# Kernel optimization log

Measured on AMD Instinct MI355X. Metric: run time of the kernel, lower is better.

The kernel has to match this reference:

```python
import jax, jax.numpy as jnp
import numpy as np

B = 1024       # batch of graphs
NUM = 512      # predicates / nodes per graph
D = 64         # embedding_dim
H = 64         # hidden_dim
E = 4096       # edges per graph (shared structure across batch)
MAIN_NUM = 10  # softmax segment [0, MAIN_NUM); sigmoid on the rest


def setup_inputs() -> dict:
    key = jax.random.key(0)
    ks = jax.random.split(key, 8)
    x = jax.random.uniform(ks[0], (B, NUM), dtype=jnp.float32)
    embedding = jax.random.normal(ks[1], (NUM, D), dtype=jnp.float32) * 0.1
    W1 = jax.random.normal(ks[2], (D, H), dtype=jnp.float32) * (1.0 / np.sqrt(D))
    b1 = jnp.zeros((H,), jnp.float32)
    W2 = jax.random.normal(ks[3], (H, H), dtype=jnp.float32) * (1.0 / np.sqrt(H))
    b2 = jnp.zeros((H,), jnp.float32)
    W3 = jax.random.normal(ks[4], (H, 1), dtype=jnp.float32) * (1.0 / np.sqrt(H))
    b3 = jnp.zeros((1,), jnp.float32)
    edge_row = jax.random.randint(ks[5], (E,), 0, NUM, dtype=jnp.int32)
    edge_col = jax.random.randint(ks[6], (E,), 0, NUM, dtype=jnp.int32)
    return {"x": x, "embedding": embedding, "W1": W1, "b1": b1,
            "W2": W2, "b2": b2, "W3": W3, "b3": b3,
            "edge_row": edge_row, "edge_col": edge_col}


def _gcn_layer(h, W, b, row, col, norm):
    # h: [B, NUM, in]; GCNConv = linear -> D^{-1/2} A D^{-1/2} aggregate -> +bias
    hW = jnp.einsum('bni,io->bno', h, W)                 # [B, NUM, out]
    msg = hW[:, row, :] * norm[None, :, None]            # [B, E, out]
    agg = jnp.zeros_like(hW).at[:, col, :].add(msg)      # scatter to targets
    return agg + b


def reference(x, embedding, W1, b1, W2, b2, W3, b3, edge_row, edge_col):
    num = x.shape[1]
    # symmetric GCN normalization (add_self_loops=False, unit edge weights)
    deg = jnp.zeros((num,), x.dtype).at[edge_col].add(1.0)
    dinv = jnp.where(deg > 0, jax.lax.rsqrt(jnp.maximum(deg, 1.0)), 0.0)
    norm = dinv[edge_row] * dinv[edge_col]               # [E]

    h = x[..., None] * embedding                         # [B, NUM, D]
    h = jax.nn.relu(_gcn_layer(h, W1, b1, edge_row, edge_col, norm))
    h = jax.nn.relu(_gcn_layer(h, W2, b2, edge_row, edge_col, norm))
    logits = _gcn_layer(h, W3, b3, edge_row, edge_col, norm)[..., 0]  # [B, NUM]

    # convert_to_confidence: softmax over multiclass segment, sigmoid elsewhere
    phi_sm = jax.nn.softmax(logits[:, :MAIN_NUM], axis=1)
    phi_sg = jax.nn.sigmoid(logits[:, MAIN_NUM:])
    return jnp.concatenate([phi_sm, phi_sg], axis=1)
```

## Files before the change

### kernel.cpp

```cpp
#include <hip/hip_runtime.h>
#include <stdint.h>

#define NB    1024
#define NUM   512
#define HD    64
#define NE    4096
#define MAIN  10
#define HBS   72

typedef __attribute__((ext_vector_type(8))) short short8;
typedef __attribute__((ext_vector_type(4))) float f32x4;

__device__ __forceinline__ short f2bf(float f) {
    uint32_t u = __float_as_uint(f);
    u += 0x7fffu + ((u >> 16) & 1u);
    return (short)(u >> 16);
}
__device__ __forceinline__ float bf2f(short s) {
    return __uint_as_float(((uint32_t)(uint16_t)s) << 16);
}

__global__ __launch_bounds__(512) void prep_all(
    const int* __restrict__ erow, const int* __restrict__ ecol,
    const float* __restrict__ emb, const float* __restrict__ W1,
    const float* __restrict__ W2,
    int* __restrict__ rsptr, int* __restrict__ colmap, int* __restrict__ epk,
    short* __restrict__ E1, short* __restrict__ W2T)
{
    const int t = threadIdx.x;
    if (blockIdx.x != 0) {
        int g = (blockIdx.x - 1) * 512 + t;
        if (g < NUM * HD) {
            int node = g >> 6, dim = g & 63;
            float acc = 0.0f;
            #pragma unroll
            for (int k = 0; k < HD; ++k) acc += emb[node * HD + k] * W1[k * HD + dim];
            E1[g] = f2bf(acc);
        } else if (g < NUM * HD + HD * HD) {
            int j = g - NUM * HD;
            int dout = j >> 6, din = j & 63;
            W2T[j] = f2bf(W2[din * HD + dout]);
        }
        return;
    }

    __shared__ int   sdeg[NUM];
    __shared__ int   aux[NUM];
    __shared__ float sdinv[NUM];
    __shared__ int   rankof[NUM];
    __shared__ int   curs[NUM];
    __shared__ int   rdeg[NUM];

    sdeg[t] = 0;
    __syncthreads();
    for (int e = t; e < NE; e += 512) atomicAdd(&sdeg[ecol[e]], 1);
    __syncthreads();
    const int deg = sdeg[t];
    const int dbin = deg < NUM ? deg : NUM - 1;
    sdinv[t] = deg > 0 ? rsqrtf((float)deg) : 0.0f;
    aux[t] = 0;
    __syncthreads();
    atomicAdd(&aux[dbin], 1);
    __syncthreads();
    for (int ofs = 1; ofs < NUM; ofs <<= 1) {
        int v = (t >= ofs) ? aux[t - ofs] : 0;
        __syncthreads();
        aux[t] += v;
        __syncthreads();
    }
    curs[t] = (t == 0) ? 0 : aux[t - 1];
    __syncthreads();
    const int r = atomicAdd(&curs[dbin], 1);
    rankof[t] = r;
    rdeg[r]   = deg;
    colmap[r] = t;
    __syncthreads();
    for (int ofs = 1; ofs < NUM; ofs <<= 1) {
        int v = (t >= ofs) ? rdeg[t - ofs] : 0;
        __syncthreads();
        rdeg[t] += v;
        __syncthreads();
    }
    rsptr[t] = (t == 0) ? 0 : rdeg[t - 1];
    if (t == NUM - 1) rsptr[NUM] = rdeg[NUM - 1];
    __syncthreads();
    const int myrank = rankof[t];
    curs[t] = (myrank == 0) ? 0 : rdeg[myrank - 1];
    __syncthreads();
    for (int e = t; e < NE; e += 512) {
        int c = ecol[e], rr = erow[e];
        int p = atomicAdd(&curs[c], 1);
        unsigned nb = (unsigned short)f2bf(sdinv[rr] * sdinv[c]);
        epk[p] = (rr << 16) | (int)nb;
    }
}

__global__ __launch_bounds__(1024, 4) void gcn_all(
    const float* __restrict__ x, const short* __restrict__ E1,
    const short* __restrict__ W2T,
    const float* __restrict__ b1, const float* __restrict__ b2,
    const float* __restrict__ W3, const float* __restrict__ b3,
    const int* __restrict__ rsptrg, const int* __restrict__ colmapg,
    const int* __restrict__ epkg,
    float* __restrict__ out)
{
    __shared__ short HA[NUM * HD];
    __shared__ short HB[NUM * HBS];
    __shared__ int   eps[NE];
    __shared__ int   sptr[513];
    __shared__ int   scm[NUM];
    __shared__ float sred[2];

    float* tv   = (float*)HB;
    float* slog = ((float*)HB) + NUM;

    const int t    = threadIdx.x;
    const int b    = blockIdx.x;
    const int lane = t & 63;
    const int wave = t >> 6;
    const int q    = lane >> 4;
    const int l15  = lane & 15;
    const int grp  = lane >> 3;
    const int dbase = (lane & 7) * 8;

    *(int4*)&eps[t * 4] = *(const int4*)&epkg[t * 4];
    if (t < 513) sptr[t] = rsptrg[t];
    if (t < NUM) scm[t] = colmapg[t];

    #pragma unroll
    for (int p = 0; p < 4; ++p) {
        int i = t + p * 1024;
        int r = i >> 3, d8 = (i & 7) * 8;
        float xr = x[b * NUM + r];
        short8 e = *(const short8*)&E1[r * HD + d8];
        short8 o;
        #pragma unroll
        for (int j = 0; j < 8; ++j) o[j] = f2bf(xr * bf2f(e[j]));
        *(short8*)&HA[r * HD + d8] = o;
    }

    float b1v[8], b2v[8], w3v[8];
    {
        f32x4 u0 = *(const f32x4*)&b1[dbase], u1 = *(const f32x4*)&b1[dbase + 4];
        f32x4 v0 = *(const f32x4*)&b2[dbase], v1 = *(const f32x4*)&b2[dbase + 4];
        f32x4 w0 = *(const f32x4*)&W3[dbase], w1 = *(const f32x4*)&W3[dbase + 4];
        #pragma unroll
        for (int j = 0; j < 4; ++j) {
            b1v[j] = u0[j]; b1v[j + 4] = u1[j];
            b2v[j] = v0[j]; b2v[j + 4] = v1[j];
            w3v[j] = w0[j]; w3v[j + 4] = w1[j];
        }
    }
    __syncthreads();

#define EDGE_MAC(pe)                                                          \
    {                                                                         \
        float n = __uint_as_float((unsigned)(pe) << 16);                      \
        uint4 hv = *(const uint4*)&HA[((unsigned)(pe) >> 16) * HD + dbase];   \
        a[0] = fmaf(n, __uint_as_float(hv.x << 16), a[0]);                    \
        a[1] = fmaf(n, __uint_as_float(hv.x & 0xffff0000u), a[1]);            \
        a[2] = fmaf(n, __uint_as_float(hv.y << 16), a[2]);                    \
        a[3] = fmaf(n, __uint_as_float(hv.y & 0xffff0000u), a[3]);            \
        a[4] = fmaf(n, __uint_as_float(hv.z << 16), a[4]);                    \
        a[5] = fmaf(n, __uint_as_float(hv.z & 0xffff0000u), a[5]);            \
        a[6] = fmaf(n, __uint_as_float(hv.w << 16), a[6]);                    \
        a[7] = fmaf(n, __uint_as_float(hv.w & 0xffff0000u), a[7]);            \
    }

    #pragma unroll 1
    for (int set = 0; set < 4; ++set) {
        int r  = set * 128 + wave * 8 + grp;
        int e0 = sptr[r], e1 = sptr[r + 1];
        int c  = scm[r];
        float a[8];
        #pragma unroll
        for (int j = 0; j < 8; ++j) a[j] = 0.0f;
        int e = e0;
        for (; e + 2 <= e1; e += 2) {
            int pe0 = eps[e], pe1 = eps[e + 1];
            EDGE_MAC(pe0);
            EDGE_MAC(pe1);
        }
        if (e < e1) { int pe0 = eps[e]; EDGE_MAC(pe0); }
        short8 o;
        #pragma unroll
        for (int j = 0; j < 8; ++j) o[j] = f2bf(fmaxf(a[j] + b1v[j], 0.0f));
        *(short8*)&HB[c * HBS + dbase] = o;
    }
    __syncthreads();

    {
        short8 bfr[2][4];
        #pragma unroll
        for (int ks = 0; ks < 2; ++ks)
            #pragma unroll
            for (int nt = 0; nt < 4; ++nt)
                bfr[ks][nt] = *(const short8*)&W2T[(nt * 16 + l15) * HD + ks * 32 + q * 8];
        f32x4 acc[2][4];
        #pragma unroll
        for (int mt = 0; mt < 2; ++mt)
            #pragma unroll
            for (int nt = 0; nt < 4; ++nt) acc[mt][nt] = (f32x4){0.f, 0.f, 0.f, 0.f};
        const int mbase = wave * 32;
        #pragma unroll
        for (int mt = 0; mt < 2; ++mt)
            #pragma unroll
            for (int ks = 0; ks < 2; ++ks) {
                short8 af = *(const short8*)&HB[(mbase + mt * 16 + l15) * HBS
                                                + ks * 32 + q * 8];
                #pragma unroll
                for (int nt = 0; nt < 4; ++nt)
                    acc[mt][nt] = __builtin_amdgcn_mfma_f32_16x16x32_bf16(
                        af, bfr[ks][nt], acc[mt][nt], 0, 0, 0);
            }
        #pragma unroll
        for (int mt = 0; mt < 2; ++mt)
            #pragma unroll
            for (int nt = 0; nt < 4; ++nt)
                #pragma unroll
                for (int i = 0; i < 4; ++i)
                    HA[(mbase + mt * 16 + q * 4 + i) * HD + nt * 16 + l15] =
                        f2bf(acc[mt][nt][i]);
    }
    __syncthreads();

    #pragma unroll 1
    for (int set = 0; set < 4; ++set) {
        int r  = set * 128 + wave * 8 + grp;
        int e0 = sptr[r], e1 = sptr[r + 1];
        int c  = scm[r];
        float a[8];
        #pragma unroll
        for (int j = 0; j < 8; ++j) a[j] = 0.0f;
        int e = e0;
        for (; e + 2 <= e1; e += 2) {
            int pe0 = eps[e], pe1 = eps[e + 1];
            EDGE_MAC(pe0);
            EDGE_MAC(pe1);
        }
        if (e < e1) { int pe0 = eps[e]; EDGE_MAC(pe0); }
        float v = 0.0f;
        #pragma unroll
        for (int j = 0; j < 8; ++j)
            v += fmaxf(a[j] + b2v[j], 0.0f) * w3v[j];
        v += __shfl_xor(v, 1, 64);
        v += __shfl_xor(v, 2, 64);
        v += __shfl_xor(v, 4, 64);
        if ((lane & 7) == 0) tv[c] = v;
    }
    __syncthreads();

    if (t < NUM) {
        int e0 = sptr[t], e1 = sptr[t + 1];
        float a = 0.0f;
        for (int e = e0; e < e1; ++e) {
            unsigned pe = (unsigned)eps[e];
            a = fmaf(__uint_as_float(pe << 16), tv[pe >> 16], a);
        }
        slog[scm[t]] = a + b3[0];
    }
    __syncthreads();

    if (t < 64) {
        float v = (t < MAIN) ? slog[t] : -1e30f;
        float m = v;
        m = fmaxf(m, __shfl_xor(m, 1, 64));
        m = fmaxf(m, __shfl_xor(m, 2, 64));
        m = fmaxf(m, __shfl_xor(m, 4, 64));
        m = fmaxf(m, __shfl_xor(m, 8, 64));
        float ev = (t < MAIN) ? __expf(v - m) : 0.0f;
        ev += __shfl_xor(ev, 1, 64);
        ev += __shfl_xor(ev, 2, 64);
        ev += __shfl_xor(ev, 4, 64);
        ev += __shfl_xor(ev, 8, 64);
        if (t == 0) { sred[0] = m; sred[1] = ev; }
    }
    __syncthreads();

    if (t < NUM) {
        float l = slog[t];
        float o = (t < MAIN) ? __expf(l - sred[0]) / sred[1]
                             : 1.0f / (1.0f + __expf(-l));
        out[b * NUM + t] = o;
    }
#undef EDGE_MAC
}

extern "C" void kernel_launch(void* const* d_in, const int* in_sizes, int n_in,
                              void* d_out, int out_size, void* d_ws, size_t ws_size,
                              hipStream_t stream) {
    const float* x    = (const float*)d_in[0];
    const float* emb  = (const float*)d_in[1];
    const float* W1   = (const float*)d_in[2];
    const float* b1   = (const float*)d_in[3];
    const float* W2   = (const float*)d_in[4];
    const float* b2   = (const float*)d_in[5];
    const float* W3   = (const float*)d_in[6];
    const float* b3   = (const float*)d_in[7];
    const int*   erow = (const int*)d_in[8];
    const int*   ecol = (const int*)d_in[9];

    char* ws = (char*)d_ws;
    int*   rsptr  = (int*)ws;
    int*   colmap = (int*)(ws + 2176);
    int*   epk    = (int*)(ws + 4224);
    short* E1     = (short*)(ws + 20608);
    short* W2T    = (short*)(ws + 86144);

    prep_all<<<73, 512, 0, stream>>>(erow, ecol, emb, W1, W2,
                                     rsptr, colmap, epk, E1, W2T);
    gcn_all<<<NB, 1024, 0, stream>>>(x, E1, W2T, b1, b2, W3, b3,
                                     rsptr, colmap, epk, (float*)d_out);
}
```

Baseline: 161.5 us.

## Fuse graph preprocessing and first-layer linear into single per-batch kernel

Removes the separate prep kernel and its workspace. Each block now builds the degree-sorted CSR edge list in shared memory, using wave-shuffle scans. It also computes the first linear layer (x*emb)@W1 per graph with MFMA, where before it scaled a precomputed emb@W1 table. W1 and W2 are read and converted to bf16 directly from global memory. This drops a kernel launch and the serialization between the two kernels, but every one of the 1024 blocks now repeats the graph preprocessing plus an extra MFMA GEMM, and it does strided uncoalesced weight loads.

```diff
diff --git a/kernel.cpp b/kernel.cpp
--- a/kernel.cpp
+++ b/kernel.cpp
@@ -20,88 +20,12 @@
     return __uint_as_float(((uint32_t)(uint16_t)s) << 16);
 }
 
-__global__ __launch_bounds__(512) void prep_all(
-    const int* __restrict__ erow, const int* __restrict__ ecol,
-    const float* __restrict__ emb, const float* __restrict__ W1,
-    const float* __restrict__ W2,
-    int* __restrict__ rsptr, int* __restrict__ colmap, int* __restrict__ epk,
-    short* __restrict__ E1, short* __restrict__ W2T)
-{
-    const int t = threadIdx.x;
-    if (blockIdx.x != 0) {
-        int g = (blockIdx.x - 1) * 512 + t;
-        if (g < NUM * HD) {
-            int node = g >> 6, dim = g & 63;
-            float acc = 0.0f;
-            #pragma unroll
-            for (int k = 0; k < HD; ++k) acc += emb[node * HD + k] * W1[k * HD + dim];
-            E1[g] = f2bf(acc);
-        } else if (g < NUM * HD + HD * HD) {
-            int j = g - NUM * HD;
-            int dout = j >> 6, din = j & 63;
-            W2T[j] = f2bf(W2[din * HD + dout]);
-        }
-        return;
-    }
-
-    __shared__ int   sdeg[NUM];
-    __shared__ int   aux[NUM];
-    __shared__ float sdinv[NUM];
-    __shared__ int   rankof[NUM];
-    __shared__ int   curs[NUM];
-    __shared__ int   rdeg[NUM];
-
-    sdeg[t] = 0;
-    __syncthreads();
-    for (int e = t; e < NE; e += 512) atomicAdd(&sdeg[ecol[e]], 1);
-    __syncthreads();
-    const int deg = sdeg[t];
-    const int dbin = deg < NUM ? deg : NUM - 1;
-    sdinv[t] = deg > 0 ? rsqrtf((float)deg) : 0.0f;
-    aux[t] = 0;
-    __syncthreads();
-    atomicAdd(&aux[dbin], 1);
-    __syncthreads();
-    for (int ofs = 1; ofs < NUM; ofs <<= 1) {
-        int v = (t >= ofs) ? aux[t - ofs] : 0;
-        __syncthreads();
-        aux[t] += v;
-        __syncthreads();
-    }
-    curs[t] = (t == 0) ? 0 : aux[t - 1];
-    __syncthreads();
-    const int r = atomicAdd(&curs[dbin], 1);
-    rankof[t] = r;
-    rdeg[r]   = deg;
-    colmap[r] = t;
-    __syncthreads();
-    for (int ofs = 1; ofs < NUM; ofs <<= 1) {
-        int v = (t >= ofs) ? rdeg[t - ofs] : 0;
-        __syncthreads();
-        rdeg[t] += v;
-        __syncthreads();
-    }
-    rsptr[t] = (t == 0) ? 0 : rdeg[t - 1];
-    if (t == NUM - 1) rsptr[NUM] = rdeg[NUM - 1];
-    __syncthreads();
-    const int myrank = rankof[t];
-    curs[t] = (myrank == 0) ? 0 : rdeg[myrank - 1];
-    __syncthreads();
-    for (int e = t; e < NE; e += 512) {
-        int c = ecol[e], rr = erow[e];
-        int p = atomicAdd(&curs[c], 1);
-        unsigned nb = (unsigned short)f2bf(sdinv[rr] * sdinv[c]);
-        epk[p] = (rr << 16) | (int)nb;
-    }
-}
-
-__global__ __launch_bounds__(1024, 4) void gcn_all(
-    const float* __restrict__ x, const short* __restrict__ E1,
-    const short* __restrict__ W2T,
+__global__ __launch_bounds__(1024, 4) void gcn_one(
+    const float* __restrict__ x, const float* __restrict__ emb,
+    const float* __restrict__ W1, const float* __restrict__ W2,
     const float* __restrict__ b1, const float* __restrict__ b2,
     const float* __restrict__ W3, const float* __restrict__ b3,
-    const int* __restrict__ rsptrg, const int* __restrict__ colmapg,
-    const int* __restrict__ epkg,
+    const int* __restrict__ erow, const int* __restrict__ ecol,
     float* __restrict__ out)
 {
     __shared__ short HA[NUM * HD];
@@ -109,34 +33,148 @@
     __shared__ int   eps[NE];
     __shared__ int   sptr[513];
     __shared__ int   scm[NUM];
+    __shared__ int   wsum[16];
     __shared__ float sred[2];
 
+    int*   sdeg = (int*)HB;
+    int*   aux  = sdeg + NUM;
+    float* sdv  = (float*)(aux + NUM);
+    int*   rnk  = (int*)(sdv + NUM);
+    int*   rdg  = rnk + NUM;
     float* tv   = (float*)HB;
     float* slog = ((float*)HB) + NUM;
 
-    const int t    = threadIdx.x;
-    const int b    = blockIdx.x;
-    const int lane = t & 63;
-    const int wave = t >> 6;
-    const int q    = lane >> 4;
-    const int l15  = lane & 15;
-    const int grp  = lane >> 3;
+    const int t     = threadIdx.x;
+    const int b     = blockIdx.x;
+    const int lane  = t & 63;
+    const int wave  = t >> 6;
+    const int q     = lane >> 4;
+    const int l15   = lane & 15;
+    const int grp   = lane >> 3;
     const int dbase = (lane & 7) * 8;
 
-    *(int4*)&eps[t * 4] = *(const int4*)&epkg[t * 4];
-    if (t < 513) sptr[t] = rsptrg[t];
-    if (t < NUM) scm[t] = colmapg[t];
-
-    #pragma unroll
-    for (int p = 0; p < 4; ++p) {
-        int i = t + p * 1024;
-        int r = i >> 3, d8 = (i & 7) * 8;
-        float xr = x[b * NUM + r];
-        short8 e = *(const short8*)&E1[r * HD + d8];
-        short8 o;
-        #pragma unroll
-        for (int j = 0; j < 8; ++j) o[j] = f2bf(xr * bf2f(e[j]));
-        *(short8*)&HA[r * HD + d8] = o;
+    if (t < NUM) { sdeg[t] = 0; aux[t] = 0; }
+    __syncthreads();
+    for (int e = t; e < NE; e += 1024) atomicAdd(&sdeg[ecol[e]], 1);
+    __syncthreads();
+    int deg = 0, dbin = 0;
+    if (t < NUM) {
+        deg  = sdeg[t];
+        dbin = deg < NUM ? deg : NUM - 1;
+        sdv[t] = deg > 0 ? rsqrtf((float)deg) : 0.0f;
+        atomicAdd(&aux[dbin], 1);
+    }
+    __syncthreads();
+    {
+        int v = (t < NUM) ? aux[t] : 0;
+        if (t < NUM) {
+            #pragma unroll
+            for (int ofs = 1; ofs < 64; ofs <<= 1) {
+                int sh = __shfl_up(v, ofs, 64);
+                if (lane >= ofs) v += sh;
+            }
+            if (lane == 63) wsum[wave] = v;
+        }
+        __syncthreads();
+        if (t == 0) {
+            int s = 0;
+            #pragma unroll
+            for (int w = 0; w < 8; ++w) { int tmp = wsum[w]; wsum[w] = s; s += tmp; }
+        }
+        __syncthreads();
+        if (t < NUM) aux[t] = v + wsum[wave];
+        __syncthreads();
+    }
+    if (t < NUM) sdeg[t] = (t == 0) ? 0 : aux[t - 1];
+    __syncthreads();
+    if (t < NUM) {
+        int r = atomicAdd(&sdeg[dbin], 1);
+        rnk[t] = r;
+        rdg[r] = deg;
+        scm[r] = t;
+    }
+    __syncthreads();
+    {
+        int dv = (t < NUM) ? rdg[t] : 0;
+        int v  = dv;
+        if (t < NUM) {
+            #pragma unroll
+            for (int ofs = 1; ofs < 64; ofs <<= 1) {
+                int sh = __shfl_up(v, ofs, 64);
+                if (lane >= ofs) v += sh;
+            }
+            if (lane == 63) wsum[wave] = v;
+        }
+        __syncthreads();
+        if (t == 0) {
+            int s = 0;
+            #pragma unroll
+            for (int w = 0; w < 8; ++w) { int tmp = wsum[w]; wsum[w] = s; s += tmp; }
+        }
+        __syncthreads();
+        if (t < NUM) {
+            int inc = v + wsum[wave];
+            sptr[t] = inc - dv;
+            if (t == NUM - 1) sptr[NUM] = inc;
+        }
+        __syncthreads();
+    }
+    if (t < NUM) aux[t] = sptr[rnk[t]];
+    __syncthreads();
+    for (int e = t; e < NE; e += 1024) {
+        int c = ecol[e], rr = erow[e];
+        int p = atomicAdd(&aux[c], 1);
+        unsigned nb = (unsigned short)f2bf(sdv[rr] * sdv[c]);
+        eps[p] = (rr << 16) | (int)nb;
+    }
+    __syncthreads();
+
+    {
+        short8 bfr[2][4];
+        #pragma unroll
+        for (int ks = 0; ks < 2; ++ks)
+            #pragma unroll
+            for (int nt = 0; nt < 4; ++nt) {
+                short8 v;
+                #pragma unroll
+                for (int j = 0; j < 8; ++j)
+                    v[j] = f2bf(W1[(ks * 32 + q * 8 + j) * HD + nt * 16 + l15]);
+                bfr[ks][nt] = v;
+            }
+        f32x4 acc[2][4];
+        #pragma unroll
+        for (int mt = 0; mt < 2; ++mt)
+            #pragma unroll
+            for (int nt = 0; nt < 4; ++nt) acc[mt][nt] = (f32x4){0.f, 0.f, 0.f, 0.f};
+        const int mbase = wave * 32;
+        #pragma unroll
+        for (int mt = 0; mt < 2; ++mt) {
+            int r = mbase + mt * 16 + l15;
+            float xr = x[b * NUM + r];
+            #pragma unroll
+            for (int ks = 0; ks < 2; ++ks) {
+                const float* ep = &emb[r * HD + ks * 32 + q * 8];
+                f32x4 e0 = *(const f32x4*)ep;
+                f32x4 e1 = *(const f32x4*)(ep + 4);
+                short8 af;
+                af[0] = f2bf(xr * e0[0]); af[1] = f2bf(xr * e0[1]);
+                af[2] = f2bf(xr * e0[2]); af[3] = f2bf(xr * e0[3]);
+                af[4] = f2bf(xr * e1[0]); af[5] = f2bf(xr * e1[1]);
+                af[6] = f2bf(xr * e1[2]); af[7] = f2bf(xr * e1[3]);
+                #pragma unroll
+                for (int nt = 0; nt < 4; ++nt)
+                    acc[mt][nt] = __builtin_amdgcn_mfma_f32_16x16x32_bf16(
+                        af, bfr[ks][nt], acc[mt][nt], 0, 0, 0);
+            }
+        }
+        #pragma unroll
+        for (int mt = 0; mt < 2; ++mt)
+            #pragma unroll
+            for (int nt = 0; nt < 4; ++nt)
+                #pragma unroll
+                for (int i = 0; i < 4; ++i)
+                    HA[(mbase + mt * 16 + q * 4 + i) * HD + nt * 16 + l15] =
+                        f2bf(acc[mt][nt][i]);
     }
 
     float b1v[8], b2v[8], w3v[8];
@@ -194,8 +232,13 @@
         #pragma unroll
         for (int ks = 0; ks < 2; ++ks)
             #pragma unroll
-            for (int nt = 0; nt < 4; ++nt)
-                bfr[ks][nt] = *(const short8*)&W2T[(nt * 16 + l15) * HD + ks * 32 + q * 8];
+            for (int nt = 0; nt < 4; ++nt) {
+                short8 v;
+                #pragma unroll
+                for (int j = 0; j < 8; ++j)
+                    v[j] = f2bf(W2[(ks * 32 + q * 8 + j) * HD + nt * 16 + l15]);
+                bfr[ks][nt] = v;
+            }
         f32x4 acc[2][4];
         #pragma unroll
         for (int mt = 0; mt < 2; ++mt)
@@ -300,15 +343,6 @@
     const int*   erow = (const int*)d_in[8];
     const int*   ecol = (const int*)d_in[9];
 
-    char* ws = (char*)d_ws;
-    int*   rsptr  = (int*)ws;
-    int*   colmap = (int*)(ws + 2176);
-    int*   epk    = (int*)(ws + 4224);
-    short* E1     = (short*)(ws + 20608);
-    short* W2T    = (short*)(ws + 86144);
-
-    prep_all<<<73, 512, 0, stream>>>(erow, ecol, emb, W1, W2,
-                                     rsptr, colmap, epk, E1, W2T);
-    gcn_all<<<NB, 1024, 0, stream>>>(x, E1, W2T, b1, b2, W3, b3,
-                                     rsptr, colmap, epk, (float*)d_out);
+    gcn_one<<<NB, 1024, 0, stream>>>(x, emb, W1, W2, b1, b2, W3, b3,
+                                     erow, ecol, (float*)d_out);
 }
```

Result: slower. 192.1 us (+19.0%).

## Pad CSR edge segments to even length and vectorize edge gathers

Applied to the files above, without the earlier changes.

Each row's edge segment is padded to an even count, with zero-filled entries that have a zero norm, so the aggregation loops can load edge words as int2 and run four edges per iteration with no odd tail. The prep kernel's scans now use wave shuffles instead of barrier-heavy shared-memory loops. The bf16 high-half unpack drops its mask, leaving the low bits as small noise. The gcn kernel reads colmap from global memory instead of staging it in LDS. The gcn kernel also loads a larger padded edge array into LDS, and the third-layer scalar loop now walks the zero padding entries too.

```diff
diff --git a/kernel.cpp b/kernel.cpp
--- a/kernel.cpp
+++ b/kernel.cpp
@@ -5,6 +5,7 @@
 #define NUM   512
 #define HD    64
 #define NE    4096
+#define NEP   4608
 #define MAIN  10
 #define HBS   72
 
@@ -46,86 +47,119 @@
 
     __shared__ int   sdeg[NUM];
     __shared__ int   aux[NUM];
-    __shared__ float sdinv[NUM];
-    __shared__ int   rankof[NUM];
-    __shared__ int   curs[NUM];
-    __shared__ int   rdeg[NUM];
-
-    sdeg[t] = 0;
+    __shared__ float sdv[NUM];
+    __shared__ int   rnk[NUM];
+    __shared__ int   rdg[NUM];
+    __shared__ int   wsum[8];
+
+    const int lane = t & 63, wv = t >> 6;
+
+    sdeg[t] = 0; aux[t] = 0;
     __syncthreads();
     for (int e = t; e < NE; e += 512) atomicAdd(&sdeg[ecol[e]], 1);
     __syncthreads();
-    const int deg = sdeg[t];
+    const int deg  = sdeg[t];
+    const int pdeg = (deg + 1) & ~1;
     const int dbin = deg < NUM ? deg : NUM - 1;
-    sdinv[t] = deg > 0 ? rsqrtf((float)deg) : 0.0f;
-    aux[t] = 0;
-    __syncthreads();
+    sdv[t] = deg > 0 ? rsqrtf((float)deg) : 0.0f;
     atomicAdd(&aux[dbin], 1);
     __syncthreads();
-    for (int ofs = 1; ofs < NUM; ofs <<= 1) {
-        int v = (t >= ofs) ? aux[t - ofs] : 0;
-        __syncthreads();
-        aux[t] += v;
-        __syncthreads();
-    }
-    curs[t] = (t == 0) ? 0 : aux[t - 1];
-    __syncthreads();
-    const int r = atomicAdd(&curs[dbin], 1);
-    rankof[t] = r;
-    rdeg[r]   = deg;
-    colmap[r] = t;
-    __syncthreads();
-    for (int ofs = 1; ofs < NUM; ofs <<= 1) {
-        int v = (t >= ofs) ? rdeg[t - ofs] : 0;
-        __syncthreads();
-        rdeg[t] += v;
-        __syncthreads();
-    }
-    rsptr[t] = (t == 0) ? 0 : rdeg[t - 1];
-    if (t == NUM - 1) rsptr[NUM] = rdeg[NUM - 1];
-    __syncthreads();
-    const int myrank = rankof[t];
-    curs[t] = (myrank == 0) ? 0 : rdeg[myrank - 1];
+    {
+        int v = aux[t];
+        #pragma unroll
+        for (int ofs = 1; ofs < 64; ofs <<= 1) {
+            int sh = __shfl_up(v, ofs, 64);
+            if (lane >= ofs) v += sh;
+        }
+        if (lane == 63) wsum[wv] = v;
+        __syncthreads();
+        if (t == 0) {
+            int s = 0;
+            #pragma unroll
+            for (int w = 0; w < 8; ++w) { int tmp = wsum[w]; wsum[w] = s; s += tmp; }
+        }
+        __syncthreads();
+        int inc = v + wsum[wv];
+        sdeg[t] = inc - ((dbin == t) ? 0 : 0);
+        aux[t]  = inc;
+        __syncthreads();
+        sdeg[t] = (t == 0) ? 0 : aux[t - 1];
+        __syncthreads();
+    }
+    {
+        int r = atomicAdd(&sdeg[dbin], 1);
+        rnk[t] = r;
+        rdg[r] = pdeg;
+        colmap[r] = t;
+    }
+    __syncthreads();
+    {
+        int dv = rdg[t], v = dv;
+        #pragma unroll
+        for (int ofs = 1; ofs < 64; ofs <<= 1) {
+            int sh = __shfl_up(v, ofs, 64);
+            if (lane >= ofs) v += sh;
+        }
+        if (lane == 63) wsum[wv] = v;
+        __syncthreads();
+        if (t == 0) {
+            int s = 0;
+            #pragma unroll
+            for (int w = 0; w < 8; ++w) { int tmp = wsum[w]; wsum[w] = s; s += tmp; }
+        }
+        __syncthreads();
+        int inc  = v + wsum[wv];
+        int excl = inc - dv;
+        rsptr[t] = excl;
+        if (t == NUM - 1) rsptr[NUM] = inc;
+        aux[t] = excl;
+        __syncthreads();
+    }
+    sdeg[t] = aux[rnk[t]];
+    __syncthreads();
+    for (int i = t; i < NEP; i += 512) epk[i] = 0;
     __syncthreads();
     for (int e = t; e < NE; e += 512) {
         int c = ecol[e], rr = erow[e];
-        int p = atomicAdd(&curs[c], 1);
-        unsigned nb = (unsigned short)f2bf(sdinv[rr] * sdinv[c]);
+        int p = atomicAdd(&sdeg[c], 1);
+        unsigned nb = (unsigned short)f2bf(sdv[rr] * sdv[c]);
         epk[p] = (rr << 16) | (int)nb;
     }
 }
 
-__global__ __launch_bounds__(1024, 4) void gcn_all(
+__global__ __launch_bounds__(1024, 4) void gcn_body(
     const float* __restrict__ x, const short* __restrict__ E1,
     const short* __restrict__ W2T,
     const float* __restrict__ b1, const float* __restrict__ b2,
     const float* __restrict__ W3, const float* __restrict__ b3,
-    const int* __restrict__ rsptrg, const int* __restrict__ colmapg,
+    const int* __restrict__ rsptrg, const int* __restrict__ colmap,
     const int* __restrict__ epkg,
     float* __restrict__ out)
 {
     __shared__ short HA[NUM * HD];
     __shared__ short HB[NUM * HBS];
-    __shared__ int   eps[NE];
+    __shared__ int   eps[NEP];
     __shared__ int   sptr[513];
-    __shared__ int   scm[NUM];
     __shared__ float sred[2];
 
     float* tv   = (float*)HB;
     float* slog = ((float*)HB) + NUM;
 
-    const int t    = threadIdx.x;
-    const int b    = blockIdx.x;
-    const int lane = t & 63;
-    const int wave = t >> 6;
-    const int q    = lane >> 4;
-    const int l15  = lane & 15;
-    const int grp  = lane >> 3;
+    const int t     = threadIdx.x;
+    const int b     = blockIdx.x;
+    const int lane  = t & 63;
+    const int wave  = t >> 6;
+    const int q     = lane >> 4;
+    const int l15   = lane & 15;
+    const int grp   = lane >> 3;
     const int dbase = (lane & 7) * 8;
 
-    *(int4*)&eps[t * 4] = *(const int4*)&epkg[t * 4];
+    {
+        const int4* g4 = (const int4*)epkg;
+        *(int4*)&eps[t * 4] = g4[t];
+        if (t < 128) *(int4*)&eps[4096 + t * 4] = g4[1024 + t];
+    }
     if (t < 513) sptr[t] = rsptrg[t];
-    if (t < NUM) scm[t] = colmapg[t];
 
     #pragma unroll
     for (int p = 0; p < 4; ++p) {
@@ -158,30 +192,33 @@
         float n = __uint_as_float((unsigned)(pe) << 16);                      \
         uint4 hv = *(const uint4*)&HA[((unsigned)(pe) >> 16) * HD + dbase];   \
         a[0] = fmaf(n, __uint_as_float(hv.x << 16), a[0]);                    \
-        a[1] = fmaf(n, __uint_as_float(hv.x & 0xffff0000u), a[1]);            \
+        a[1] = fmaf(n, __uint_as_float(hv.x), a[1]);                          \
         a[2] = fmaf(n, __uint_as_float(hv.y << 16), a[2]);                    \
-        a[3] = fmaf(n, __uint_as_float(hv.y & 0xffff0000u), a[3]);            \
+        a[3] = fmaf(n, __uint_as_float(hv.y), a[3]);                          \
         a[4] = fmaf(n, __uint_as_float(hv.z << 16), a[4]);                    \
-        a[5] = fmaf(n, __uint_as_float(hv.z & 0xffff0000u), a[5]);            \
+        a[5] = fmaf(n, __uint_as_float(hv.z), a[5]);                          \
         a[6] = fmaf(n, __uint_as_float(hv.w << 16), a[6]);                    \
-        a[7] = fmaf(n, __uint_as_float(hv.w & 0xffff0000u), a[7]);            \
+        a[7] = fmaf(n, __uint_as_float(hv.w), a[7]);                          \
     }
 
     #pragma unroll 1
     for (int set = 0; set < 4; ++set) {
         int r  = set * 128 + wave * 8 + grp;
         int e0 = sptr[r], e1 = sptr[r + 1];
-        int c  = scm[r];
+        int c  = colmap[r];
         float a[8];
         #pragma unroll
         for (int j = 0; j < 8; ++j) a[j] = 0.0f;
         int e = e0;
-        for (; e + 2 <= e1; e += 2) {
-            int pe0 = eps[e], pe1 = eps[e + 1];
-            EDGE_MAC(pe0);
-            EDGE_MAC(pe1);
-        }
-        if (e < e1) { int pe0 = eps[e]; EDGE_MAC(pe0); }
+        for (; e + 4 <= e1; e += 4) {
+            int2 pa = *(const int2*)&eps[e];
+            int2 pb = *(const int2*)&eps[e + 2];
+            EDGE_MAC(pa.x); EDGE_MAC(pa.y); EDGE_MAC(pb.x); EDGE_MAC(pb.y);
+        }
+        if (e < e1) {
+            int2 pa = *(const int2*)&eps[e];
+            EDGE_MAC(pa.x); EDGE_MAC(pa.y);
+        }
         short8 o;
         #pragma unroll
         for (int j = 0; j < 8; ++j) o[j] = f2bf(fmaxf(a[j] + b1v[j], 0.0f));
@@ -228,17 +265,20 @@
     for (int set = 0; set < 4; ++set) {
         int r  = set * 128 + wave * 8 + grp;
         int e0 = sptr[r], e1 = sptr[r + 1];
-        int c  = scm[r];
+        int c  = colmap[r];
         float a[8];
         #pragma unroll
         for (int j = 0; j < 8; ++j) a[j] = 0.0f;
         int e = e0;
-        for (; e + 2 <= e1; e += 2) {
-            int pe0 = eps[e], pe1 = eps[e + 1];
-            EDGE_MAC(pe0);
-            EDGE_MAC(pe1);
-        }
-        if (e < e1) { int pe0 = eps[e]; EDGE_MAC(pe0); }
+        for (; e + 4 <= e1; e += 4) {
+            int2 pa = *(const int2*)&eps[e];
+            int2 pb = *(const int2*)&eps[e + 2];
+            EDGE_MAC(pa.x); EDGE_MAC(pa.y); EDGE_MAC(pb.x); EDGE_MAC(pb.y);
+        }
+        if (e < e1) {
+            int2 pa = *(const int2*)&eps[e];
+            EDGE_MAC(pa.x); EDGE_MAC(pa.y);
+        }
         float v = 0.0f;
         #pragma unroll
         for (int j = 0; j < 8; ++j)
@@ -257,7 +297,7 @@
             unsigned pe = (unsigned)eps[e];
             a = fmaf(__uint_as_float(pe << 16), tv[pe >> 16], a);
         }
-        slog[scm[t]] = a + b3[0];
+        slog[colmap[t]] = a + b3[0];
     }
     __syncthreads();
 
@@ -304,11 +344,11 @@
     int*   rsptr  = (int*)ws;
     int*   colmap = (int*)(ws + 2176);
     int*   epk    = (int*)(ws + 4224);
-    short* E1     = (short*)(ws + 20608);
-    short* W2T    = (short*)(ws + 86144);
+    short* E1     = (short*)(ws + 22656);
+    short* W2T    = (short*)(ws + 88192);
 
     prep_all<<<73, 512, 0, stream>>>(erow, ecol, emb, W1, W2,
                                      rsptr, colmap, epk, E1, W2T);
-    gcn_all<<<NB, 1024, 0, stream>>>(x, E1, W2T, b1, b2, W3, b3,
-                                     rsptr, colmap, epk, (float*)d_out);
-}
+    gcn_body<<<NB, 1024, 0, stream>>>(x, E1, W2T, b1, b2, W3, b3,
+                                      rsptr, colmap, epk, (float*)d_out);
+}
```

After: 157.4 us. -2.5%, faster.
